# Kernel tuning notes

Measured on AMD Instinct MI355X. Metric: run time of the kernel, lower is better.

The kernel has to match this reference:

```python
import jax, jax.numpy as jnp
import numpy as np
from jax.scipy.linalg import expm

B, D, CUT, LAYERS = 256, 4, 10, 4
K = D * (D - 1) // 2            # beamsplitter pairs per interferometer
P = 4 * K + 6 * D               # params per CVQNN layer (=48 for D=4)


def _ops(c):
    a = jnp.diag(jnp.sqrt(jnp.arange(1, c, dtype=jnp.float32)), k=1).astype(jnp.complex64)
    return a, a.T, jnp.arange(c, dtype=jnp.float32)


def _apply_single(state, U, m):
    t = jnp.tensordot(state, U, axes=((m + 1,), (1,)))
    return jnp.moveaxis(t, -1, m + 1)


def _apply_two(state, U4, i, j):
    t = jnp.tensordot(state, U4, axes=((i + 1, j + 1), (2, 3)))
    return jnp.moveaxis(t, (-2, -1), (i + 1, j + 1))


def _mul_diag(state, diag, m, d, c):
    return state * diag.reshape((1,) * (m + 1) + (c,) + (1,) * (d - m - 1))


def _interferometer(state, th, ph, vph, a, adag, n, d, c):
    pairs = [(i, j) for i in range(d) for j in range(i + 1, d)]
    Aab = jnp.kron(adag, a)  # adag_i a_j on a mode pair

    def gen(t, p):
        tc = t.astype(jnp.complex64)
        pc = p.astype(jnp.complex64)
        return tc * (jnp.exp(1j * pc) * Aab - jnp.exp(-1j * pc) * Aab.conj().T)

    U = jax.vmap(expm)(jax.vmap(gen)(th, ph)).reshape(len(pairs), c, c, c, c)
    for k, (i, j) in enumerate(pairs):
        state = _apply_two(state, U[k], i, j)
    nc = n.astype(jnp.complex64)
    for m in range(d):
        state = _mul_diag(state, jnp.exp(1j * vph[m].astype(jnp.complex64) * nc), m, d, c)
    return state


def _layer(state, w, a, adag, n, d, c):
    k = d * (d - 1) // 2
    o = 0
    th1 = w[o:o + k]; o += k
    ph1 = w[o:o + k]; o += k
    vp1 = w[o:o + d]; o += d
    rsq = w[o:o + d]; o += d
    th2 = w[o:o + k]; o += k
    ph2 = w[o:o + k]; o += k
    vp2 = w[o:o + d]; o += d
    rd = w[o:o + d]; o += d
    phd = w[o:o + d]; o += d
    kap = w[o:o + d]

    state = _interferometer(state, th1, ph1, vp1, a, adag, n, d, c)
    # per-mode squeezing S(r) = exp(r/2 (a^2 - adag^2))
    Ss = jax.vmap(lambda r: expm(0.5 * r.astype(jnp.complex64) * (a @ a - adag @ adag)))(rsq)
    for m in range(d):
        state = _apply_single(state, Ss[m], m)
    state = _interferometer(state, th2, ph2, vp2, a, adag, n, d, c)
    # per-mode displacement D(alpha)
    alpha = rd.astype(jnp.complex64) * jnp.exp(1j * phd.astype(jnp.complex64))
    Ds = jax.vmap(lambda al: expm(al * adag - jnp.conj(al) * a))(alpha)
    for m in range(d):
        state = _apply_single(state, Ds[m], m)
    # per-mode Kerr: diag(exp(i kappa n^2))
    nc = n.astype(jnp.complex64)
    for m in range(d):
        state = _mul_diag(state, jnp.exp(1j * kap[m].astype(jnp.complex64) * nc * nc), m, d, c)
    return state


def _forward(inputs, weights):
    d, c = D, CUT
    a, adag, n = _ops(c)
    # BatchPrepare: per mode |psi> = Displacement(r, 0) Squeezing(0.5, pi/2) |0>
    z = 0.5j  # r=0.5, phi=pi/2
    S0 = expm(0.5 * (jnp.conj(z) * (a @ a) - z * (adag @ adag)))
    psi0 = S0[:, 0]  # S |0>
    Dm = jax.vmap(lambda r: expm(r.astype(jnp.complex64) * (adag - a)))(inputs.reshape(-1))
    psi = (Dm @ psi0).reshape(inputs.shape[0], d, c)  # [B, d, c]
    # tensor product over modes -> [B, c, ..., c]
    state = psi[:, 0]
    for m in range(1, d):
        state = jnp.einsum('b...,bc->b...c', state, psi[:, m])
    for l in range(LAYERS):
        state = _layer(state, weights[l], a, adag, n, d, c)
    probs = jnp.abs(state) ** 2  # no normalization (Config(normalize=False))
    outs = [jnp.sum(_mul_diag(probs, n, m, d, c), axis=tuple(range(1, d + 1))) for m in range(d)]
    return jnp.stack(outs, axis=1)  # [B, modes] mean photon numbers


def setup_inputs() -> dict:
    key = jax.random.key(0)
    k1, k2 = jax.random.split(key)
    inputs = 0.3 * jax.random.normal(k1, (B, D), dtype=jnp.float32)
    cvqnn_weights = 0.1 * jax.random.normal(k2, (LAYERS, P), dtype=jnp.float32)
    return {"inputs": inputs, "cvqnn_weights": cvqnn_weights, "batch_size": B}


def reference(inputs, cvqnn_weights, batch_size):
    assert inputs.shape[0] == batch_size
    return _forward(inputs, cvqnn_weights)
```

## Files before the change

### kernel.cpp

```cpp
#include <hip/hip_runtime.h>
#include <hip/hip_bf16.h>

#define CUT 10
#define NB 256
#define NLAYERS 4
#define WSTRIDE 48

#define R_DM 0
#define R_SQ 1024
#define R_DS 1040
#define R_BS 1056
#define NRSLOTS 1968

#define F0 1110
#define F1 111
#define F2 11
#define F3 1
#define ST_PHYS 11100

#define LUT_A  0
#define LUT_B  60
#define LUT_C  120
#define LUT_I  234
#define LUT_S  253
#define LUT_IS 259
#define LUT_K  260
#define LUT_N  300

typedef __hip_bfloat16 bf16;

__device__ __forceinline__ float readv(const void* p, int i, int isf32) {
  if (isf32) return ((const float*)p)[i];
  return __bfloat162float(((const bf16*)p)[i]);
}

__device__ __forceinline__ void rmacL(float2& a, float2 mm, float2 v) {
  asm("v_pk_fma_f32 %0, %1, %2, %0 op_sel:[0,0,0] op_sel_hi:[0,1,1]"
      : "+v"(a) : "v"(mm), "v"(v));
}
__device__ __forceinline__ void rmacH(float2& a, float2 mm, float2 v) {
  asm("v_pk_fma_f32 %0, %1, %2, %0 op_sel:[1,0,0] op_sel_hi:[1,1,1]"
      : "+v"(a) : "v"(mm), "v"(v));
}

__device__ __forceinline__ float2 cmul(float2 u, float2 v) {
  float2 d;
  asm("v_pk_mul_f32 %0, %1, %2 op_sel:[0,0] op_sel_hi:[0,1]\n\t"
      "v_pk_fma_f32 %0, %1, %2, %0 op_sel:[1,1,0] op_sel_hi:[1,0,1] neg_lo:[1,0,0]"
      : "=&v"(d) : "v"(u), "v"(v));
  return d;
}

__device__ __forceinline__ float2 loF(const float4& q) { return make_float2(q.x, q.y); }
__device__ __forceinline__ float2 hiF(const float4& q) { return make_float2(q.z, q.w); }

__device__ const signed char g_perm[16][3] = {
  {18,-1,-1},{19,-1,-1},{16, 0,-1},{17, 1,-1},{20,36,-1},{21,37,-1},
  {14, 6,34},{15, 7,35},{22,30,-1},{23,31,-1},{12, 8, 4},{13, 9, 5},
  {24,28,32},{25,29,33},{10,26, 2},{11,27, 3}
};

__global__ void sniff_dtype(const void* p, int n_elems, int* flag) {
  __shared__ float red[256];
  const unsigned short* h = (const unsigned short*)p;
  int t = threadIdx.x;
  float mx = 0.f;
  for (int i = t; i < n_elems; i += 256) {
    unsigned short u = h[i];
    bf16 bv = *(const bf16*)&u;
    float v = fabsf(__bfloat162float(bv));
    if (!(v < 1e30f)) v = 1e30f;
    mx = fmaxf(mx, v);
  }
  red[t] = mx;
  __syncthreads();
  for (int off = 128; off > 0; off >>= 1) {
    if (t < off) red[t] = fmaxf(red[t], red[t + off]);
    __syncthreads();
  }
  if (t == 0) *flag = (red[0] > 1000.f) ? 1 : 0;
}

__global__ void build_gens(float* rslots, float2* s0, const void* inp,
                           const void* w, const int* flag) {
  int s = blockIdx.x;
  int t = threadIdx.x;
  if (t >= 100) return;
  int isf32 = *flag;
  int i = t / 10, j = t % 10;
  if (s == NRSLOTS) {
    float2 val = make_float2(0.f, 0.f);
    if (j == i + 2)      { float c = sqrtf((float)((i+1)*(i+2))); val.y = -0.25f*c; }
    else if (i == j + 2) { float c = sqrtf((float)((j+1)*(j+2))); val.y = -0.25f*c; }
    s0[t] = val;
    return;
  }
  float val = 0.f;
  if (s < R_SQ) {
    float r = readv(inp, s, isf32);
    if (i == j + 1)      val =  r * sqrtf((float)(j+1));
    else if (j == i + 1) val = -r * sqrtf((float)(i+1));
  } else if (s < R_DS) {
    int k = s - R_SQ; int l = k >> 2; int m = k & 3;
    float r = readv(w, l*WSTRIDE + 16 + m, isf32);
    if (j == i + 2)      val =  0.5f*r*sqrtf((float)((i+1)*(i+2)));
    else if (i == j + 2) val = -0.5f*r*sqrtf((float)((j+1)*(j+2)));
  } else if (s < R_BS) {
    int k = s - R_DS; int l = k >> 2; int m = k & 3;
    float rd = readv(w, l*WSTRIDE + 36 + m, isf32);
    if (i == j + 1)      val =  rd * sqrtf((float)(j+1));
    else if (j == i + 1) val = -rd * sqrtf((float)(i+1));
  } else {
    int rel = s - R_BS;
    int g = rel / 19; int N = rel % 19;
    int l = g / 12; int hf = (g % 12) / 6; int p = g % 6;
    float th = readv(w, l*WSTRIDE + (hf ? 20 : 0) + p, isf32);
    int lo = max(0, N - 9), hi = min(9, N);
    int d = hi - lo + 1;
    if (i < d && j < d) {
      if (i == j + 1)      val =  th * sqrtf((float)((lo + j + 1) * (N - lo - j)));
      else if (j == i + 1) val = -th * sqrtf((float)((lo + i + 1) * (N - lo - i)));
    }
  }
  rslots[(size_t)s * 100 + t] = val;
}

__global__ void expm_real(float* rslots) {
  __shared__ float T[100], Pm[100], R[100];
  __shared__ float rowsum[10];
  __shared__ int sshift;
  int s = blockIdx.x, t = threadIdx.x;
  int i = t / 10, j = t % 10;
  float* G = rslots + (size_t)s * 100;
  if (t < 100) T[t] = G[t];
  __syncthreads();
  if (t < 10) {
    float sum = 0.f;
    for (int c = 0; c < 10; ++c) sum += fabsf(T[t*10+c]);
    rowsum[t] = sum;
  }
  __syncthreads();
  if (t == 0) {
    float nm = 0.f;
    for (int r = 0; r < 10; ++r) nm = fmaxf(nm, rowsum[r]);
    int sc = 0;
    if (!(nm < 1e6f)) sc = 0;
    else if (nm > 0.25f) sc = (int)ceilf(log2f(nm * 4.f));
    sshift = min(max(sc, 0), 40);
  }
  __syncthreads();
  int sh = sshift;
  float scl = ldexpf(1.f, -sh);
  if (t < 100) {
    float z = T[t] * scl;
    T[t] = z; Pm[t] = z;
    R[t] = z + (i == j ? 1.f : 0.f);
  }
  __syncthreads();
  for (int k = 2; k <= 12; ++k) {
    float acc = 0.f;
    if (t < 100) {
      for (int c = 0; c < 10; ++c) acc += Pm[i*10+c] * T[c*10+j];
      acc *= 1.f / (float)k;
    }
    __syncthreads();
    if (t < 100) { Pm[t] = acc; R[t] += acc; }
    __syncthreads();
  }
  for (int q = 0; q < sh; ++q) {
    float acc = 0.f;
    if (t < 100) {
      for (int c = 0; c < 10; ++c) acc += R[i*10+c] * R[c*10+j];
    }
    __syncthreads();
    if (t < 100) R[t] = acc;
    __syncthreads();
  }
  if (t < 100) G[t] = R[t];
}

__global__ void expm_cplx(float2* G) {
  __shared__ float2 T[100], P[100], R[100];
  __shared__ float rowsum[10];
  __shared__ int sshift;
  int t = threadIdx.x;
  int i = t / 10, j = t % 10;
  if (t < 100) T[t] = G[t];
  __syncthreads();
  if (t < 10) {
    float sum = 0.f;
    for (int c = 0; c < 10; ++c) { float2 z = T[t*10+c]; sum += fabsf(z.x) + fabsf(z.y); }
    rowsum[t] = sum;
  }
  __syncthreads();
  if (t == 0) {
    float nm = 0.f;
    for (int r = 0; r < 10; ++r) nm = fmaxf(nm, rowsum[r]);
    int sc = 0;
    if (!(nm < 1e6f)) sc = 0;
    else if (nm > 0.25f) sc = (int)ceilf(log2f(nm * 4.f));
    sshift = min(max(sc, 0), 40);
  }
  __syncthreads();
  int sh = sshift;
  float scl = ldexpf(1.f, -sh);
  if (t < 100) {
    float2 z = T[t]; z.x *= scl; z.y *= scl;
    T[t] = z; P[t] = z;
    R[t] = make_float2(z.x + (i == j ? 1.f : 0.f), z.y);
  }
  __syncthreads();
  for (int k = 2; k <= 12; ++k) {
    float2 acc = make_float2(0.f, 0.f);
    if (t < 100) {
      for (int c = 0; c < 10; ++c) {
        float2 a = P[i*10+c], b = T[c*10+j];
        acc.x += a.x*b.x - a.y*b.y;
        acc.y += a.x*b.y + a.y*b.x;
      }
      float inv = 1.f / (float)k;
      acc.x *= inv; acc.y *= inv;
    }
    __syncthreads();
    if (t < 100) { P[t] = acc; R[t].x += acc.x; R[t].y += acc.y; }
    __syncthreads();
  }
  for (int q = 0; q < sh; ++q) {
    float2 acc = make_float2(0.f, 0.f);
    if (t < 100) {
      for (int c = 0; c < 10; ++c) {
        float2 a = R[i*10+c], b = R[c*10+j];
        acc.x += a.x*b.x - a.y*b.y;
        acc.y += a.x*b.y + a.y*b.x;
      }
    }
    __syncthreads();
    if (t < 100) R[t] = acc;
    __syncthreads();
  }
  if (t < 100) G[t] = R[t];
}

__device__ __forceinline__ void gate_fs(const void* w, int isf32, int l, int half,
                                        int g, float& f0, float& f1, float& f3,
                                        float& fdc) {
  int po = l*WSTRIDE + (half ? 26 : 6);
  int vo = l*WSTRIDE + (half ? 32 : 12);
  f0 = 0.f; f1 = 0.f; f3 = 0.f;
  switch (g) {
    case 0: fdc = readv(w, po+0, isf32) - readv(w, po+1, isf32); break;
    case 1: fdc = readv(w, po+1, isf32) - readv(w, po+2, isf32); break;
    case 2: f0 = -readv(w, po+3, isf32); fdc = readv(w, po+2, isf32); break;
    case 3: fdc = readv(w, po+3, isf32) - readv(w, po+4, isf32); break;
    case 4: f1 = -readv(w, po+5, isf32); fdc = readv(w, po+4, isf32); break;
    default: {
      float vp0 = readv(w, vo+0, isf32), vp1 = readv(w, vo+1, isf32);
      float vp2 = readv(w, vo+2, isf32), vp3 = readv(w, vo+3, isf32);
      if (half) {
        vp0 -= readv(w, l*WSTRIDE+40+0, isf32);
        vp1 -= readv(w, l*WSTRIDE+40+1, isf32);
        vp2 -= readv(w, l*WSTRIDE+40+2, isf32);
        vp3 -= readv(w, l*WSTRIDE+40+3, isf32);
      }
      f0 = vp0; f1 = vp1; f3 = vp3;
      fdc = vp2 + readv(w, po+5, isf32) - vp3;
    }
  }
}

#define LOADQ(DST, P) do { _Pragma("unroll") \
  for (int q_ = 0; q_ < 5; ++q_) DST[q_] = Uq[(P)*5 + q_]; } while (0)

#define BS_PAIR(UA, R0)                                                        \
  {                                                                            \
    float2 a0 = make_float2(0.f,0.f), a1 = make_float2(0.f,0.f);               \
    _Pragma("unroll")                                                          \
    for (int j = 0; j < 5; ++j) if (2*j < sd) {                                \
      const float2 m0 = (j==0)?loF(UA[0]):(j==1)?hiF(UA[0]):(j==2)?loF(UA[1])  \
                        :(j==3)?hiF(UA[1]):loF(UA[2]);                         \
      const float2 m1 = (j==0)?hiF(UA[2]):(j==1)?loF(UA[3]):(j==2)?hiF(UA[3])  \
                        :(j==3)?loF(UA[4]):hiF(UA[4]);                         \
      rmacL(a0, m0, v[2*j]); rmacH(a0, m0, v[2*j+1]);                          \
      rmacL(a1, m1, v[2*j]); rmacH(a1, m1, v[2*j+1]);                          \
    }                                                                          \
    a0 = cmul(a0, rot); rot = cmul(rot, step);                                 \
    base[(R0)*se] = a0;                                                        \
    if ((R0) + 1 < sd) {                                                       \
      a1 = cmul(a1, rot); rot = cmul(rot, step);                               \
      base[((R0)+1)*se] = a1;                                                  \
    }                                                                          \
  }

template<int sI, int sJ, int sA, int sB, bool INROT>
__device__ __forceinline__ void bs_chunk(
    float2* st, const float* __restrict__ U, int sd,
    int hi10, int lo10, int lo, int N,
    float2 rot, float2 step, float2 ir, float2 istep)
{
  constexpr int se = sI - sJ;
  float2* base = st + hi10*sA + lo10*sB + lo*sI + (N - lo)*sJ;
  float2 v[10];
#pragma unroll
  for (int k = 0; k < 10; ++k) {
    if (k < sd) {
      float2 tv = base[k*se];
      if (INROT) { tv = cmul(tv, ir); ir = cmul(ir, istep); }
      v[k] = tv;
    } else {
      v[k] = make_float2(0.f, 0.f);
    }
  }
  const float4* Uq = (const float4*)U;
  float4 ua[5], ub[5];
  LOADQ(ua, 0);
#pragma unroll
  for (int p = 0; p < 5; p += 2) {
    if (2*p < sd) {
      if (2*p + 2 < sd) LOADQ(ub, p + 1);
      BS_PAIR(ua, 2*p);
    }
    if (2*p + 2 < sd) {
      if (2*p + 4 < sd) LOADQ(ua, p + 2);
      BS_PAIR(ub, 2*p + 2);
    }
  }
}

template<int sI, int sJ, int sA, int sB, bool INROT>
__device__ __forceinline__ void bs_gate(
    float2* st, const float* __restrict__ Ub, const float2* __restrict__ lut,
    int g, int lane, int ch0, int ch1, int ch2)
{
  const float2 step  = lut[LUT_S + g];
  const float2 istep = INROT ? lut[LUT_IS] : make_float2(1.f, 0.f);
#pragma unroll
  for (int r = 0; r < 3; ++r) {
    const int c = (r == 0) ? ch0 : (r == 1) ? ch1 : ch2;
    if (c >= 0) {
      int N = c >> 1;
      int spec = ((c & 1) << 6) + lane;
      if (spec < 100) {
        int lo = max(0, N - 9);
        const int sd = __builtin_amdgcn_readfirstlane(min(9, N) - lo + 1);
        int hi10 = spec / 10, lo10 = spec % 10;
        float2 rot = cmul(cmul(lut[LUT_A + g*10 + hi10], lut[LUT_B + g*10 + lo10]),
                          lut[LUT_C + g*19 + N]);
        float2 ir = INROT ? lut[LUT_I + N] : make_float2(1.f, 0.f);
        bs_chunk<sI,sJ,sA,sB,INROT>(st, Ub + N*100, sd, hi10, lo10, lo, N,
                                    rot, step, ir, istep);
      }
    }
  }
}

#define SM_PAIR(UA, R0)                                                        \
  {                                                                            \
    float2 a0 = make_float2(0.f,0.f), a1 = make_float2(0.f,0.f);               \
    _Pragma("unroll")                                                          \
    for (int j = 0; j < 5; ++j) {                                              \
      const float2 m0 = (j==0)?loF(UA[0]):(j==1)?hiF(UA[0]):(j==2)?loF(UA[1])  \
                        :(j==3)?hiF(UA[1]):loF(UA[2]);                         \
      const float2 m1 = (j==0)?hiF(UA[2]):(j==1)?loF(UA[3]):(j==2)?hiF(UA[3])  \
                        :(j==3)?loF(UA[4]):hiF(UA[4]);                         \
      rmacL(a0, m0, v[2*j]); rmacH(a0, m0, v[2*j+1]);                          \
      rmacL(a1, m1, v[2*j]); rmacH(a1, m1, v[2*j+1]);                          \
    }                                                                          \
    if (KERR) {                                                                \
      a0 = cmul(a0, cmul(kb, lut[LUT_K + 30 + (R0)]));                         \
      a1 = cmul(a1, cmul(kb, lut[LUT_K + 30 + (R0) + 1]));                     \
    }                                                                          \
    base[(R0)*sM] = a0;                                                        \
    base[((R0)+1)*sM] = a1;                                                    \
  }

template<int sM, int pA, int pB, int pC, bool KERR>
__device__ __forceinline__ void sm_gate(
    float2* st, const float* __restrict__ U, const float2* __restrict__ lut,
    bool smv, int q0, int q1, int q2)
{
  if (!smv) return;
  float2* base = st + q0*pA + q1*pB + q2*pC;
  float2 kb = make_float2(1.f, 0.f);
  if (KERR) kb = cmul(cmul(lut[LUT_K + q0], lut[LUT_K + 10 + q1]),
                      lut[LUT_K + 20 + q2]);
  float2 v[10];
#pragma unroll
  for (int k = 0; k < 10; ++k) v[k] = base[k*sM];
  const float4* Uq = (const float4*)U;
  float4 ua[5], ub[5];
  LOADQ(ua, 0);
#pragma unroll
  for (int p = 0; p < 5; p += 2) {
    {
      if (p < 4) LOADQ(ub, p + 1);
      SM_PAIR(ua, 2*p);
    }
    if (p + 1 < 5) {
      if (p + 2 < 5) LOADQ(ua, p + 2);
      SM_PAIR(ub, 2*(p + 1));
    }
  }
}

__global__ __launch_bounds__(1024, 4)
void fused_circuit(
    const float* __restrict__ rslots, const float2* __restrict__ s0,
    const void* __restrict__ w, const int* __restrict__ flag,
    float* __restrict__ out)
{
  __shared__ float2 st[ST_PHYS];
  __shared__ __align__(16) float smU[3200];
  __shared__ __align__(16) float bsU[2*1900];
  __shared__ float2 lut[LUT_N];
  __shared__ float2 psi[4][10];
  __shared__ float redw[64];
  const int b = blockIdx.x, t = threadIdx.x;
  const int wv = t >> 6, lane = t & 63;
  const int isf32 = *flag;

  const int ch0 = g_perm[wv][0], ch1 = g_perm[wv][1], ch2 = g_perm[wv][2];
  const bool smv = (t < 1000);
  const int q0 = t / 100, q1 = (t / 10) % 10, q2 = t % 10;

  if (t < 40) {
    int m = t / 10, r = t % 10;
    const float* Dmr = rslots + (size_t)(R_DM + b*4 + m) * 100;
    float2 acc = make_float2(0.f, 0.f);
    for (int c = 0; c < 10; ++c) {
      float a = Dmr[r*10 + c];
      float2 vv = s0[c * 10];
      acc.x += a * vv.x;
      acc.y += a * vv.y;
    }
    psi[m][r] = acc;
  }
  for (int i = t; i < 800; i += 1024)
    ((float4*)smU)[i] = ((const float4*)(rslots + (size_t)R_SQ * 100))[i];
  for (int i = t; i < 475; i += 1024)
    ((float4*)bsU)[i] = ((const float4*)(rslots + (size_t)R_BS * 100))[i];
  __syncthreads();
  for (int e = t; e < 10000; e += 1024) {
    int ph = e + e/10 + e/100;
    float2 z  = psi[0][e/1000];
    float2 w1 = psi[1][(e/100)%10];
    float2 r1 = make_float2(z.x*w1.x - z.y*w1.y, z.x*w1.y + z.y*w1.x);
    float2 w2 = psi[2][(e/10)%10];
    float2 r2 = make_float2(r1.x*w2.x - r1.y*w2.y, r1.x*w2.y + r1.y*w2.x);
    float2 w3 = psi[3][e%10];
    st[ph] = make_float2(r2.x*w3.x - r2.y*w3.y, r2.x*w3.y + r2.y*w3.x);
  }
  __syncthreads();

  float4 pf;
  auto pf_load = [&](int next) {
    if (next < 48 && t < 475)
      pf = ((const float4*)(rslots + (size_t)(R_BS + next*19) * 100))[t];
  };
  auto pf_store = [&](int next) {
    if (next < 48 && t < 475)
      ((float4*)(bsU + (next & 1) * 1900))[t] = pf;
  };

#pragma unroll 1
  for (int l = 0; l < NLAYERS; ++l) {
#pragma unroll 1
    for (int half = 0; half < 2; ++half) {
      const int g6 = l*12 + half*6;

      {
        const int po = l*WSTRIDE + (half ? 26 : 6);
        if (t < LUT_N) {
          float ang = 0.f;
          if (t < 120) {
            int isB = (t >= 60);
            int id = isB ? t - 60 : t;
            int g = id / 10, q = id % 10;
            float f0, f1, f3, fd;
            gate_fs(w, isf32, l, half, g, f0, f1, f3, fd);
            ang = (isB ? f1 : f0) * (float)q;
          } else if (t < 234) {
            int id = t - 120; int g = id / 19, N = id % 19;
            float f0, f1, f3, fd;
            gate_fs(w, isf32, l, half, g, f0, f1, f3, fd);
            int lo = max(0, N - 9);
            ang = f3 * (float)N + fd * (float)lo;
          } else if (t < 253) {
            int N = t - 234; int lo = max(0, N - 9);
            ang = -readv(w, po + 0, isf32) * (float)lo;
          } else if (t < 259) {
            int g = t - 253;
            float f0, f1, f3, fd;
            gate_fs(w, isf32, l, half, g, f0, f1, f3, fd);
            ang = fd;
          } else if (t == 259) {
            ang = -readv(w, po + 0, isf32);
          } else {
            int id = t - 260; int m = id / 10, q = id % 10;
            if (half) {
              float kap = readv(w, l*WSTRIDE + 44 + m, isf32);
              float pd  = readv(w, l*WSTRIDE + 40 + m, isf32);
              ang = kap * (float)(q*q) + pd * (float)q;
            }
          }
          float sn, cs; sincosf(ang, &sn, &cs);
          lut[t] = make_float2(cs, sn);
        }
        __syncthreads();
      }

      pf_load(g6+1);
      bs_gate<F0,F1,F2,F3,true >(st, bsU+((g6+0)&1)*1900, lut, 0, lane, ch0,ch1,ch2);
      pf_store(g6+1);
      __syncthreads();
      pf_load(g6+2);
      bs_gate<F0,F2,F1,F3,false>(st, bsU+((g6+1)&1)*1900, lut, 1, lane, ch0,ch1,ch2);
      pf_store(g6+2);
      __syncthreads();
      pf_load(g6+3);
      bs_gate<F0,F3,F1,F2,false>(st, bsU+((g6+2)&1)*1900, lut, 2, lane, ch0,ch1,ch2);
      pf_store(g6+3);
      __syncthreads();
      pf_load(g6+4);
      bs_gate<F1,F2,F0,F3,false>(st, bsU+((g6+3)&1)*1900, lut, 3, lane, ch0,ch1,ch2);
      pf_store(g6+4);
      __syncthreads();
      pf_load(g6+5);
      bs_gate<F1,F3,F0,F2,false>(st, bsU+((g6+4)&1)*1900, lut, 4, lane, ch0,ch1,ch2);
      pf_store(g6+5);
      __syncthreads();
      pf_load(g6+6);
      bs_gate<F2,F3,F0,F1,false>(st, bsU+((g6+5)&1)*1900, lut, 5, lane, ch0,ch1,ch2);
      pf_store(g6+6);
      __syncthreads();

      const int ub_ = (half == 0) ? (l*4) : (16 + l*4);
      sm_gate<F0,F1,F2,F3,false>(st, smU+(ub_+0)*100, lut, smv, q0,q1,q2);
      __syncthreads();
      sm_gate<F1,F0,F2,F3,false>(st, smU+(ub_+1)*100, lut, smv, q0,q1,q2);
      __syncthreads();
      sm_gate<F2,F0,F1,F3,false>(st, smU+(ub_+2)*100, lut, smv, q0,q1,q2);
      __syncthreads();
      if (half)
        sm_gate<F3,F0,F1,F2,true >(st, smU+(ub_+3)*100, lut, smv, q0,q1,q2);
      else
        sm_gate<F3,F0,F1,F2,false>(st, smU+(ub_+3)*100, lut, smv, q0,q1,q2);
      __syncthreads();
    }
  }

  float a0 = 0.f, a1 = 0.f, a2 = 0.f, a3 = 0.f;
  for (int e = t; e < 10000; e += 1024) {
    int ph = e + e/10 + e/100;
    float2 z = st[ph];
    float pz = z.x*z.x + z.y*z.y;
    a0 += pz * (float)(e/1000);
    a1 += pz * (float)((e/100)%10);
    a2 += pz * (float)((e/10)%10);
    a3 += pz * (float)(e%10);
  }
  for (int off2 = 32; off2 > 0; off2 >>= 1) {
    a0 += __shfl_down(a0, off2, 64);
    a1 += __shfl_down(a1, off2, 64);
    a2 += __shfl_down(a2, off2, 64);
    a3 += __shfl_down(a3, off2, 64);
  }
  if (lane == 0) {
    redw[wv*4+0] = a0; redw[wv*4+1] = a1;
    redw[wv*4+2] = a2; redw[wv*4+3] = a3;
  }
  __syncthreads();
  if (t < 4) {
    float s = 0.f;
    for (int ww = 0; ww < 16; ++ww) s += redw[ww*4 + t];
    out[b*4 + t] = s;
  }
}

extern "C" void kernel_launch(void* const* d_in, const int* in_sizes, int n_in,
                              void* d_out, int out_size, void* d_ws, size_t ws_size,
                              hipStream_t stream) {
  const void* inp = d_in[0];
  const void* w   = d_in[1];
  float* out = (float*)d_out;
  int*    flag   = (int*)d_ws;
  float2* s0     = (float2*)((char*)d_ws + 16);
  float*  rslots = (float*)((char*)d_ws + 1024);

  sniff_dtype<<<dim3(1), dim3(256), 0, stream>>>(inp, in_sizes[0], flag);
  build_gens<<<dim3(NRSLOTS + 1), dim3(128), 0, stream>>>(rslots, s0, inp, w, flag);
  expm_real<<<dim3(NRSLOTS), dim3(128), 0, stream>>>(rslots);
  expm_cplx<<<dim3(1), dim3(128), 0, stream>>>(s0);
  fused_circuit<<<dim3(NB), dim3(1024), 0, stream>>>(rslots, s0, w, flag, out);
}
```

Baseline: 349.4 us.

## Read gate matrices from global memory via scalar loads and double-buffer the LUT

The gate unitaries are no longer staged in LDS, either as a full preload or as a double-buffered prefetch. Each wave now reads them straight from global memory through a wave-uniform pointer, so they can be fetched with scalar loads and fed to the packed FMAs as SGPR operands. The per-half LUT build is moved into the previous half's final sync phase using a double-buffered LUT, which removes one barrier per half. The beamsplitter gate now loads the state for all three chunks up front and uses a step-squared rotation to shorten dependency chains. In exchange it relies on scalar cache hits and raises register pressure.

```diff
diff --git a/kernel.cpp b/kernel.cpp
--- a/kernel.cpp
+++ b/kernel.cpp
@@ -25,7 +25,10 @@
 #define LUT_S  253
 #define LUT_IS 259
 #define LUT_K  260
-#define LUT_N  300
+#define LUT_S2 300
+#define LUT_IS2 306
+#define LUT_N  307
+#define LUT_PAD 320
 
 typedef __hip_bfloat16 bf16;
 
@@ -34,13 +37,13 @@
   return __bfloat162float(((const bf16*)p)[i]);
 }
 
-__device__ __forceinline__ void rmacL(float2& a, float2 mm, float2 v) {
+__device__ __forceinline__ void rmacLs(float2& a, float2 mm, float2 v) {
   asm("v_pk_fma_f32 %0, %1, %2, %0 op_sel:[0,0,0] op_sel_hi:[0,1,1]"
-      : "+v"(a) : "v"(mm), "v"(v));
-}
-__device__ __forceinline__ void rmacH(float2& a, float2 mm, float2 v) {
+      : "+v"(a) : "s"(mm), "v"(v));
+}
+__device__ __forceinline__ void rmacHs(float2& a, float2 mm, float2 v) {
   asm("v_pk_fma_f32 %0, %1, %2, %0 op_sel:[1,0,0] op_sel_hi:[1,1,1]"
-      : "+v"(a) : "v"(mm), "v"(v));
+      : "+v"(a) : "s"(mm), "v"(v));
 }
 
 __device__ __forceinline__ float2 cmul(float2 u, float2 v) {
@@ -51,8 +54,12 @@
   return d;
 }
 
-__device__ __forceinline__ float2 loF(const float4& q) { return make_float2(q.x, q.y); }
-__device__ __forceinline__ float2 hiF(const float4& q) { return make_float2(q.z, q.w); }
+__device__ __forceinline__ const float* uni(const float* p) {
+  unsigned long long v = (unsigned long long)p;
+  unsigned lo = __builtin_amdgcn_readfirstlane((unsigned)v);
+  unsigned hi = __builtin_amdgcn_readfirstlane((unsigned)(v >> 32));
+  return (const float*)(((unsigned long long)hi << 32) | lo);
+}
 
 __device__ const signed char g_perm[16][3] = {
   {18,-1,-1},{19,-1,-1},{16, 0,-1},{17, 1,-1},{20,36,-1},{21,37,-1},
@@ -268,137 +275,175 @@
   }
 }
 
-#define LOADQ(DST, P) do { _Pragma("unroll") \
-  for (int q_ = 0; q_ < 5; ++q_) DST[q_] = Uq[(P)*5 + q_]; } while (0)
-
-#define BS_PAIR(UA, R0)                                                        \
-  {                                                                            \
-    float2 a0 = make_float2(0.f,0.f), a1 = make_float2(0.f,0.f);               \
-    _Pragma("unroll")                                                          \
-    for (int j = 0; j < 5; ++j) if (2*j < sd) {                                \
-      const float2 m0 = (j==0)?loF(UA[0]):(j==1)?hiF(UA[0]):(j==2)?loF(UA[1])  \
-                        :(j==3)?hiF(UA[1]):loF(UA[2]);                         \
-      const float2 m1 = (j==0)?hiF(UA[2]):(j==1)?loF(UA[3]):(j==2)?hiF(UA[3])  \
-                        :(j==3)?loF(UA[4]):hiF(UA[4]);                         \
-      rmacL(a0, m0, v[2*j]); rmacH(a0, m0, v[2*j+1]);                          \
-      rmacL(a1, m1, v[2*j]); rmacH(a1, m1, v[2*j+1]);                          \
-    }                                                                          \
-    a0 = cmul(a0, rot); rot = cmul(rot, step);                                 \
-    base[(R0)*se] = a0;                                                        \
-    if ((R0) + 1 < sd) {                                                       \
-      a1 = cmul(a1, rot); rot = cmul(rot, step);                               \
-      base[((R0)+1)*se] = a1;                                                  \
-    }                                                                          \
-  }
+__device__ __forceinline__ void build_lut(float2* lb, const void* w, int isf32,
+                                          int l, int half, int t) {
+  const int po = l*WSTRIDE + (half ? 26 : 6);
+  if (t < LUT_N) {
+    float ang = 0.f;
+    if (t < 120) {
+      int isB = (t >= 60);
+      int id = isB ? t - 60 : t;
+      int g = id / 10, q = id % 10;
+      float f0, f1, f3, fd;
+      gate_fs(w, isf32, l, half, g, f0, f1, f3, fd);
+      ang = (isB ? f1 : f0) * (float)q;
+    } else if (t < 234) {
+      int id = t - 120; int g = id / 19, N = id % 19;
+      float f0, f1, f3, fd;
+      gate_fs(w, isf32, l, half, g, f0, f1, f3, fd);
+      int lo = max(0, N - 9);
+      ang = f3 * (float)N + fd * (float)lo;
+    } else if (t < 253) {
+      int N = t - 234; int lo = max(0, N - 9);
+      ang = -readv(w, po + 0, isf32) * (float)lo;
+    } else if (t < 259) {
+      int g = t - 253;
+      float f0, f1, f3, fd;
+      gate_fs(w, isf32, l, half, g, f0, f1, f3, fd);
+      ang = fd;
+    } else if (t == 259) {
+      ang = -readv(w, po + 0, isf32);
+    } else if (t < 300) {
+      int id = t - 260; int m = id / 10, q = id % 10;
+      if (half) {
+        float kap = readv(w, l*WSTRIDE + 44 + m, isf32);
+        float pd  = readv(w, l*WSTRIDE + 40 + m, isf32);
+        ang = kap * (float)(q*q) + pd * (float)q;
+      }
+    } else if (t < 306) {
+      int g = t - 300;
+      float f0, f1, f3, fd;
+      gate_fs(w, isf32, l, half, g, f0, f1, f3, fd);
+      ang = 2.f * fd;
+    } else {
+      ang = -2.f * readv(w, po + 0, isf32);
+    }
+    float sn, cs; sincosf(ang, &sn, &cs);
+    lb[t] = make_float2(cs, sn);
+  }
+}
 
 template<int sI, int sJ, int sA, int sB, bool INROT>
-__device__ __forceinline__ void bs_chunk(
-    float2* st, const float* __restrict__ U, int sd,
-    int hi10, int lo10, int lo, int N,
-    float2 rot, float2 step, float2 ir, float2 istep)
+__device__ __forceinline__ void bs_gate(
+    float2* st, const float* __restrict__ Ugate, const float2* __restrict__ L,
+    int g, int lane, int ch0, int ch1, int ch2)
 {
   constexpr int se = sI - sJ;
-  float2* base = st + hi10*sA + lo10*sB + lo*sI + (N - lo)*sJ;
-  float2 v[10];
-#pragma unroll
-  for (int k = 0; k < 10; ++k) {
-    if (k < sd) {
-      float2 tv = base[k*se];
-      if (INROT) { tv = cmul(tv, ir); ir = cmul(ir, istep); }
-      v[k] = tv;
-    } else {
-      v[k] = make_float2(0.f, 0.f);
-    }
-  }
-  const float4* Uq = (const float4*)U;
-  float4 ua[5], ub[5];
-  LOADQ(ua, 0);
-#pragma unroll
-  for (int p = 0; p < 5; p += 2) {
-    if (2*p < sd) {
-      if (2*p + 2 < sd) LOADQ(ub, p + 1);
-      BS_PAIR(ua, 2*p);
-    }
-    if (2*p + 2 < sd) {
-      if (2*p + 4 < sd) LOADQ(ua, p + 2);
-      BS_PAIR(ub, 2*p + 2);
-    }
-  }
-}
-
-template<int sI, int sJ, int sA, int sB, bool INROT>
-__device__ __forceinline__ void bs_gate(
-    float2* st, const float* __restrict__ Ub, const float2* __restrict__ lut,
-    int g, int lane, int ch0, int ch1, int ch2)
-{
-  const float2 step  = lut[LUT_S + g];
-  const float2 istep = INROT ? lut[LUT_IS] : make_float2(1.f, 0.f);
+  const float2 step1 = L[LUT_S + g];
+  const float2 step2 = L[LUT_S2 + g];
+  const int chs[3] = {ch0, ch1, ch2};
+  float2 v[3][10];
+  float2* cb[3]; int csd[3]; bool cok[3]; int cN[3]; int chi[3], clo[3];
 #pragma unroll
   for (int r = 0; r < 3; ++r) {
-    const int c = (r == 0) ? ch0 : (r == 1) ? ch1 : ch2;
+    int c = chs[r];
+    csd[r] = 0; cok[r] = false; cb[r] = st; cN[r] = 0; chi[r] = 0; clo[r] = 0;
     if (c >= 0) {
       int N = c >> 1;
       int spec = ((c & 1) << 6) + lane;
-      if (spec < 100) {
-        int lo = max(0, N - 9);
-        const int sd = __builtin_amdgcn_readfirstlane(min(9, N) - lo + 1);
-        int hi10 = spec / 10, lo10 = spec % 10;
-        float2 rot = cmul(cmul(lut[LUT_A + g*10 + hi10], lut[LUT_B + g*10 + lo10]),
-                          lut[LUT_C + g*19 + N]);
-        float2 ir = INROT ? lut[LUT_I + N] : make_float2(1.f, 0.f);
-        bs_chunk<sI,sJ,sA,sB,INROT>(st, Ub + N*100, sd, hi10, lo10, lo, N,
-                                    rot, step, ir, istep);
-      }
-    }
-  }
-}
-
-#define SM_PAIR(UA, R0)                                                        \
-  {                                                                            \
-    float2 a0 = make_float2(0.f,0.f), a1 = make_float2(0.f,0.f);               \
-    _Pragma("unroll")                                                          \
-    for (int j = 0; j < 5; ++j) {                                              \
-      const float2 m0 = (j==0)?loF(UA[0]):(j==1)?hiF(UA[0]):(j==2)?loF(UA[1])  \
-                        :(j==3)?hiF(UA[1]):loF(UA[2]);                         \
-      const float2 m1 = (j==0)?hiF(UA[2]):(j==1)?loF(UA[3]):(j==2)?hiF(UA[3])  \
-                        :(j==3)?loF(UA[4]):hiF(UA[4]);                         \
-      rmacL(a0, m0, v[2*j]); rmacH(a0, m0, v[2*j+1]);                          \
-      rmacL(a1, m1, v[2*j]); rmacH(a1, m1, v[2*j+1]);                          \
-    }                                                                          \
-    if (KERR) {                                                                \
-      a0 = cmul(a0, cmul(kb, lut[LUT_K + 30 + (R0)]));                         \
-      a1 = cmul(a1, cmul(kb, lut[LUT_K + 30 + (R0) + 1]));                     \
-    }                                                                          \
-    base[(R0)*sM] = a0;                                                        \
-    base[((R0)+1)*sM] = a1;                                                    \
-  }
+      int lo = max(0, N - 9);
+      csd[r] = __builtin_amdgcn_readfirstlane(min(9, N) - lo + 1);
+      cN[r] = N;
+      cok[r] = (spec < 100);
+      int hi10 = spec / 10, lo10 = spec % 10;
+      chi[r] = hi10; clo[r] = lo10;
+      cb[r] = st + hi10*sA + lo10*sB + lo*sI + (N - lo)*sJ;
+    }
+  }
+#pragma unroll
+  for (int r = 0; r < 3; ++r) {
+    int sd = csd[r];
+#pragma unroll
+    for (int k = 0; k < 10; ++k) {
+      if (k < sd && cok[r]) v[r][k] = cb[r][k*se];
+      else                  v[r][k] = make_float2(0.f, 0.f);
+    }
+  }
+#pragma unroll
+  for (int r = 0; r < 3; ++r) {
+    if (csd[r] > 0) {
+      const int N = cN[r];
+      const int sd = csd[r];
+      float2 rot0 = cmul(cmul(L[LUT_A + g*10 + chi[r]], L[LUT_B + g*10 + clo[r]]),
+                         L[LUT_C + g*19 + N]);
+      float2 rot1 = cmul(rot0, step1);
+      if (INROT) {
+        float2 ir0 = L[LUT_I + N];
+        float2 ir1 = cmul(ir0, L[LUT_IS]);
+        float2 is2 = L[LUT_IS2];
+#pragma unroll
+        for (int k = 0; k < 10; k += 2) {
+          v[r][k]   = cmul(v[r][k],   ir0); ir0 = cmul(ir0, is2);
+          v[r][k+1] = cmul(v[r][k+1], ir1); ir1 = cmul(ir1, is2);
+        }
+      }
+      const float4* Uq = (const float4*)uni(Ugate + N*100);
+      float2* base = cb[r];
+      const bool ok = cok[r];
+#pragma unroll
+      for (int p = 0; p < 5; ++p) if (2*p < sd) {
+        float4 u0 = Uq[p*5+0], u1 = Uq[p*5+1], u2 = Uq[p*5+2],
+               u3 = Uq[p*5+3], u4 = Uq[p*5+4];
+        float2 a0 = make_float2(0.f,0.f), a1 = make_float2(0.f,0.f);
+#pragma unroll
+        for (int j = 0; j < 5; ++j) if (2*j < sd) {
+          const float2 m0 = (j==0)?make_float2(u0.x,u0.y):(j==1)?make_float2(u0.z,u0.w)
+                           :(j==2)?make_float2(u1.x,u1.y):(j==3)?make_float2(u1.z,u1.w)
+                           :make_float2(u2.x,u2.y);
+          const float2 m1 = (j==0)?make_float2(u2.z,u2.w):(j==1)?make_float2(u3.x,u3.y)
+                           :(j==2)?make_float2(u3.z,u3.w):(j==3)?make_float2(u4.x,u4.y)
+                           :make_float2(u4.z,u4.w);
+          rmacLs(a0, m0, v[r][2*j]); rmacHs(a0, m0, v[r][2*j+1]);
+          rmacLs(a1, m1, v[r][2*j]); rmacHs(a1, m1, v[r][2*j+1]);
+        }
+        a0 = cmul(a0, rot0);
+        if (ok) base[(2*p)*se] = a0;
+        if (2*p + 1 < sd) {
+          a1 = cmul(a1, rot1);
+          if (ok) base[(2*p+1)*se] = a1;
+        }
+        rot0 = cmul(rot0, step2);
+        rot1 = cmul(rot1, step2);
+      }
+    }
+  }
+}
 
 template<int sM, int pA, int pB, int pC, bool KERR>
 __device__ __forceinline__ void sm_gate(
-    float2* st, const float* __restrict__ U, const float2* __restrict__ lut,
+    float2* st, const float* __restrict__ Ug, const float2* __restrict__ L,
     bool smv, int q0, int q1, int q2)
 {
+  const float4* Uq = (const float4*)uni(Ug);
   if (!smv) return;
   float2* base = st + q0*pA + q1*pB + q2*pC;
   float2 kb = make_float2(1.f, 0.f);
-  if (KERR) kb = cmul(cmul(lut[LUT_K + q0], lut[LUT_K + 10 + q1]),
-                      lut[LUT_K + 20 + q2]);
+  if (KERR) kb = cmul(cmul(L[LUT_K + q0], L[LUT_K + 10 + q1]), L[LUT_K + 20 + q2]);
   float2 v[10];
 #pragma unroll
   for (int k = 0; k < 10; ++k) v[k] = base[k*sM];
-  const float4* Uq = (const float4*)U;
-  float4 ua[5], ub[5];
-  LOADQ(ua, 0);
-#pragma unroll
-  for (int p = 0; p < 5; p += 2) {
-    {
-      if (p < 4) LOADQ(ub, p + 1);
-      SM_PAIR(ua, 2*p);
-    }
-    if (p + 1 < 5) {
-      if (p + 2 < 5) LOADQ(ua, p + 2);
-      SM_PAIR(ub, 2*(p + 1));
-    }
+#pragma unroll
+  for (int p = 0; p < 5; ++p) {
+    float4 u0 = Uq[p*5+0], u1 = Uq[p*5+1], u2 = Uq[p*5+2],
+           u3 = Uq[p*5+3], u4 = Uq[p*5+4];
+    float2 a0 = make_float2(0.f,0.f), a1 = make_float2(0.f,0.f);
+#pragma unroll
+    for (int j = 0; j < 5; ++j) {
+      const float2 m0 = (j==0)?make_float2(u0.x,u0.y):(j==1)?make_float2(u0.z,u0.w)
+                       :(j==2)?make_float2(u1.x,u1.y):(j==3)?make_float2(u1.z,u1.w)
+                       :make_float2(u2.x,u2.y);
+      const float2 m1 = (j==0)?make_float2(u2.z,u2.w):(j==1)?make_float2(u3.x,u3.y)
+                       :(j==2)?make_float2(u3.z,u3.w):(j==3)?make_float2(u4.x,u4.y)
+                       :make_float2(u4.z,u4.w);
+      rmacLs(a0, m0, v[2*j]); rmacHs(a0, m0, v[2*j+1]);
+      rmacLs(a1, m1, v[2*j]); rmacHs(a1, m1, v[2*j+1]);
+    }
+    if (KERR) {
+      a0 = cmul(a0, cmul(kb, L[LUT_K + 30 + 2*p]));
+      a1 = cmul(a1, cmul(kb, L[LUT_K + 30 + 2*p + 1]));
+    }
+    base[(2*p)*sM]   = a0;
+    base[(2*p+1)*sM] = a1;
   }
 }
 
@@ -409,16 +454,17 @@
     float* __restrict__ out)
 {
   __shared__ float2 st[ST_PHYS];
-  __shared__ __align__(16) float smU[3200];
-  __shared__ __align__(16) float bsU[2*1900];
-  __shared__ float2 lut[LUT_N];
+  __shared__ float2 lut[2][LUT_PAD];
   __shared__ float2 psi[4][10];
   __shared__ float redw[64];
   const int b = blockIdx.x, t = threadIdx.x;
   const int wv = t >> 6, lane = t & 63;
   const int isf32 = *flag;
 
-  const int ch0 = g_perm[wv][0], ch1 = g_perm[wv][1], ch2 = g_perm[wv][2];
+  const int wvu = __builtin_amdgcn_readfirstlane(wv);
+  const int ch0 = __builtin_amdgcn_readfirstlane((int)g_perm[wvu][0]);
+  const int ch1 = __builtin_amdgcn_readfirstlane((int)g_perm[wvu][1]);
+  const int ch2 = __builtin_amdgcn_readfirstlane((int)g_perm[wvu][2]);
   const bool smv = (t < 1000);
   const int q0 = t / 100, q1 = (t / 10) % 10, q2 = t % 10;
 
@@ -434,10 +480,7 @@
     }
     psi[m][r] = acc;
   }
-  for (int i = t; i < 800; i += 1024)
-    ((float4*)smU)[i] = ((const float4*)(rslots + (size_t)R_SQ * 100))[i];
-  for (int i = t; i < 475; i += 1024)
-    ((float4*)bsU)[i] = ((const float4*)(rslots + (size_t)R_BS * 100))[i];
+  build_lut(lut[0], w, isf32, 0, 0, t);
   __syncthreads();
   for (int e = t; e < 10000; e += 1024) {
     int ph = e + e/10 + e/100;
@@ -451,100 +494,47 @@
   }
   __syncthreads();
 
-  float4 pf;
-  auto pf_load = [&](int next) {
-    if (next < 48 && t < 475)
-      pf = ((const float4*)(rslots + (size_t)(R_BS + next*19) * 100))[t];
-  };
-  auto pf_store = [&](int next) {
-    if (next < 48 && t < 475)
-      ((float4*)(bsU + (next & 1) * 1900))[t] = pf;
-  };
-
+  int par = 0;
 #pragma unroll 1
   for (int l = 0; l < NLAYERS; ++l) {
 #pragma unroll 1
     for (int half = 0; half < 2; ++half) {
       const int g6 = l*12 + half*6;
-
-      {
-        const int po = l*WSTRIDE + (half ? 26 : 6);
-        if (t < LUT_N) {
-          float ang = 0.f;
-          if (t < 120) {
-            int isB = (t >= 60);
-            int id = isB ? t - 60 : t;
-            int g = id / 10, q = id % 10;
-            float f0, f1, f3, fd;
-            gate_fs(w, isf32, l, half, g, f0, f1, f3, fd);
-            ang = (isB ? f1 : f0) * (float)q;
-          } else if (t < 234) {
-            int id = t - 120; int g = id / 19, N = id % 19;
-            float f0, f1, f3, fd;
-            gate_fs(w, isf32, l, half, g, f0, f1, f3, fd);
-            int lo = max(0, N - 9);
-            ang = f3 * (float)N + fd * (float)lo;
-          } else if (t < 253) {
-            int N = t - 234; int lo = max(0, N - 9);
-            ang = -readv(w, po + 0, isf32) * (float)lo;
-          } else if (t < 259) {
-            int g = t - 253;
-            float f0, f1, f3, fd;
-            gate_fs(w, isf32, l, half, g, f0, f1, f3, fd);
-            ang = fd;
-          } else if (t == 259) {
-            ang = -readv(w, po + 0, isf32);
-          } else {
-            int id = t - 260; int m = id / 10, q = id % 10;
-            if (half) {
-              float kap = readv(w, l*WSTRIDE + 44 + m, isf32);
-              float pd  = readv(w, l*WSTRIDE + 40 + m, isf32);
-              ang = kap * (float)(q*q) + pd * (float)q;
-            }
-          }
-          float sn, cs; sincosf(ang, &sn, &cs);
-          lut[t] = make_float2(cs, sn);
-        }
-        __syncthreads();
-      }
-
-      pf_load(g6+1);
-      bs_gate<F0,F1,F2,F3,true >(st, bsU+((g6+0)&1)*1900, lut, 0, lane, ch0,ch1,ch2);
-      pf_store(g6+1);
-      __syncthreads();
-      pf_load(g6+2);
-      bs_gate<F0,F2,F1,F3,false>(st, bsU+((g6+1)&1)*1900, lut, 1, lane, ch0,ch1,ch2);
-      pf_store(g6+2);
-      __syncthreads();
-      pf_load(g6+3);
-      bs_gate<F0,F3,F1,F2,false>(st, bsU+((g6+2)&1)*1900, lut, 2, lane, ch0,ch1,ch2);
-      pf_store(g6+3);
-      __syncthreads();
-      pf_load(g6+4);
-      bs_gate<F1,F2,F0,F3,false>(st, bsU+((g6+3)&1)*1900, lut, 3, lane, ch0,ch1,ch2);
-      pf_store(g6+4);
-      __syncthreads();
-      pf_load(g6+5);
-      bs_gate<F1,F3,F0,F2,false>(st, bsU+((g6+4)&1)*1900, lut, 4, lane, ch0,ch1,ch2);
-      pf_store(g6+5);
-      __syncthreads();
-      pf_load(g6+6);
-      bs_gate<F2,F3,F0,F1,false>(st, bsU+((g6+5)&1)*1900, lut, 5, lane, ch0,ch1,ch2);
-      pf_store(g6+6);
+      const float2* L = lut[par];
+      const float* Ubs = rslots + (size_t)(R_BS + g6*19) * 100;
+
+      bs_gate<F0,F1,F2,F3,true >(st, Ubs + 0*1900, L, 0, lane, ch0,ch1,ch2);
+      __syncthreads();
+      bs_gate<F0,F2,F1,F3,false>(st, Ubs + 1*1900, L, 1, lane, ch0,ch1,ch2);
+      __syncthreads();
+      bs_gate<F0,F3,F1,F2,false>(st, Ubs + 2*1900, L, 2, lane, ch0,ch1,ch2);
+      __syncthreads();
+      bs_gate<F1,F2,F0,F3,false>(st, Ubs + 3*1900, L, 3, lane, ch0,ch1,ch2);
+      __syncthreads();
+      bs_gate<F1,F3,F0,F2,false>(st, Ubs + 4*1900, L, 4, lane, ch0,ch1,ch2);
+      __syncthreads();
+      bs_gate<F2,F3,F0,F1,false>(st, Ubs + 5*1900, L, 5, lane, ch0,ch1,ch2);
       __syncthreads();
 
       const int ub_ = (half == 0) ? (l*4) : (16 + l*4);
-      sm_gate<F0,F1,F2,F3,false>(st, smU+(ub_+0)*100, lut, smv, q0,q1,q2);
-      __syncthreads();
-      sm_gate<F1,F0,F2,F3,false>(st, smU+(ub_+1)*100, lut, smv, q0,q1,q2);
-      __syncthreads();
-      sm_gate<F2,F0,F1,F3,false>(st, smU+(ub_+2)*100, lut, smv, q0,q1,q2);
+      const float* Usm = rslots + (size_t)(R_SQ + ub_) * 100;
+      sm_gate<F0,F1,F2,F3,false>(st, Usm + 0*100, L, smv, q0,q1,q2);
+      __syncthreads();
+      sm_gate<F1,F0,F2,F3,false>(st, Usm + 1*100, L, smv, q0,q1,q2);
+      __syncthreads();
+      sm_gate<F2,F0,F1,F3,false>(st, Usm + 2*100, L, smv, q0,q1,q2);
       __syncthreads();
       if (half)
-        sm_gate<F3,F0,F1,F2,true >(st, smU+(ub_+3)*100, lut, smv, q0,q1,q2);
+        sm_gate<F3,F0,F1,F2,true >(st, Usm + 3*100, L, smv, q0,q1,q2);
       else
-        sm_gate<F3,F0,F1,F2,false>(st, smU+(ub_+3)*100, lut, smv, q0,q1,q2);
-      __syncthreads();
+        sm_gate<F3,F0,F1,F2,false>(st, Usm + 3*100, L, smv, q0,q1,q2);
+      if (!(l == NLAYERS-1 && half == 1)) {
+        int nl = (half == 1) ? l + 1 : l;
+        int nh = half ^ 1;
+        build_lut(lut[par ^ 1], w, isf32, nl, nh, t);
+      }
+      __syncthreads();
+      par ^= 1;
     }
   }
 
```

Result: slower. 702.2 us (+101.0%).
